# Optimization experiments

Hardware: AMD Instinct MI355X
Metric: run time of the kernel (lower is better)

Reference implementation:

```python
import jax, jax.numpy as jnp
import numpy as np
from jax import lax

BN_EPS = 1e-5

@jax.custom_vjp
def ste_sign(x):
    # Binarize to {-1, +1} (sign; 0 maps to 0 like torch.sign, negligible measure)
    return jnp.sign(x)

def _ste_fwd(x):
    return jnp.sign(x), x

def _ste_bwd(x, g):
    # Straight-through estimator: pass gradient where |x| <= 1
    return (g * (jnp.abs(x) <= 1.0).astype(g.dtype),)

ste_sign.defvjp(_ste_fwd, _ste_bwd)

def bin_conv3x3(x, w, stride=1):
    # Binarize both activations and weights, then 3x3 conv, padding=1, no bias
    xb = ste_sign(x)
    wb = ste_sign(w)
    return lax.conv_general_dilated(
        xb, wb, window_strides=(stride, stride), padding=((1, 1), (1, 1)),
        dimension_numbers=('NCHW', 'OIHW', 'NCHW'))

def batchnorm_inf(x, gamma, beta, mean, var):
    # Inference-mode BatchNorm2d over channel dim (axis=1)
    scale = gamma * lax.rsqrt(var + BN_EPS)
    shift = beta - mean * scale
    return x * scale[None, :, None, None] + shift[None, :, None, None]

def hardtanh(x):
    # SelfTanh modeled as hardtanh (standard BNN activation with STE-style grad)
    return jnp.clip(x, -1.0, 1.0)

def setup_inputs() -> dict:
    key = jax.random.key(0)
    ks = jax.random.split(key, 3)
    N, C, H, W = 64, 256, 56, 56
    x = jax.random.normal(ks[0], (N, C, H, W), dtype=jnp.float32)
    w1 = jax.random.normal(ks[1], (C, C, 3, 3), dtype=jnp.float32) * (1.0 / math_sqrt(9 * C))
    w2 = jax.random.normal(ks[2], (C, C, 3, 3), dtype=jnp.float32) * (1.0 / math_sqrt(9 * C))
    ones = jnp.ones((C,), jnp.float32)
    zeros = jnp.zeros((C,), jnp.float32)
    return {
        'x': x,
        'w1': w1, 'g1': ones, 'b1': zeros, 'm1': zeros, 'v1': ones,
        'w2': w2, 'g2': ones, 'b2': zeros, 'm2': zeros, 'v2': ones,
    }

def math_sqrt(v):
    return float(np.sqrt(v))

def reference(x, w1, g1, b1, m1, v1, w2, g2, b2, m2, v2):
    residual = x
    out = bin_conv3x3(x, w1, stride=1)
    out = batchnorm_inf(out, g1, b1, m1, v1)
    out = hardtanh(out)
    out = bin_conv3x3(out, w2, stride=1)
    out = batchnorm_inf(out, g2, b2, m2, v2)
    out = out + residual
    out = hardtanh(out)
    return out
```

## Files before the change

kernel.cpp:

```cpp
#include <hip/hip_runtime.h>
#include <stdint.h>


#define NB 64
#define C  256
#define H  56
#define W  56
#define HP 58
#define PPIX 272
#define SLOT (HP * PPIX)
#define OST 272
#define FST 116

typedef int v4i __attribute__((ext_vector_type(4)));

__global__ __launch_bounds__(256)
void pack_x_kernel(const float* __restrict__ x, int8_t* __restrict__ Aq) {
    const int h = blockIdx.x, n = blockIdx.y;
    const int w  = threadIdx.x & 63;
    const int cq = threadIdx.x >> 6;

    __shared__ int8_t st[56 * OST];

    const float* xp = x + (((size_t)n * C + cq * 64) * H + h) * W + w;
#pragma unroll
    for (int i = 0; i < 16; ++i) {
        uint32_t u = 0;
#pragma unroll
        for (int b = 0; b < 4; ++b) {
            float v = (w < 56) ? xp[(size_t)(i * 4 + b) * (H * W)] : 0.0f;
            uint32_t t = (v < 0.0f) ? 0xFFu : ((v != 0.0f) ? 1u : 0u);
            u |= t << (8 * b);
        }
        if (w < 56)
            *(uint32_t*)(st + w * OST + cq * 64 + i * 4) = u;
    }
    __syncthreads();
    int8_t* dst = Aq + (((size_t)n * HP + h + 1) * HP + 1) * C;
    for (int idx = threadIdx.x; idx < 56 * 16; idx += 256) {
        int pix = idx >> 4, c16 = idx & 15;
        *(v4i*)(dst + (size_t)pix * C + c16 * 16) =
            *(const v4i*)(st + pix * OST + c16 * 16);
    }
}

__global__ __launch_bounds__(64)
void pack_w_kernel(const float* __restrict__ wa, const float* __restrict__ wb,
                   int8_t* __restrict__ B1, int8_t* __restrict__ B2) {
    const int kstep = blockIdx.x;
    const int nfrag = blockIdx.y;
    const float* wsrc = blockIdx.z ? wb : wa;
    int8_t* dst       = blockIdx.z ? B2 : B1;
    const int lane = threadIdx.x, quad = lane >> 4, l16 = lane & 15;
    const int co = nfrag * 16 + l16;
    uint32_t pk[4];
#pragma unroll
    for (int d = 0; d < 4; ++d) {
        uint32_t u = 0;
#pragma unroll
        for (int bb = 0; bb < 4; ++bb) {
            int k = kstep * 64 + quad * 16 + d * 4 + bb;
            int tap = k >> 8, ci = k & 255;
            float v = wsrc[((size_t)co * C + ci) * 9 + tap];
            uint32_t t = (v < 0.0f) ? 0xFFu : ((v != 0.0f) ? 1u : 0u);
            u |= t << (8 * bb);
        }
        pk[d] = u;
    }
    uint4 st; st.x = pk[0]; st.y = pk[1]; st.z = pk[2]; st.w = pk[3];
    *(uint4*)(dst + ((size_t)(nfrag * 36 + kstep) * 64 + lane) * 16) = st;
}

__global__ __launch_bounds__(256)
void halo_zero_kernel(int8_t* __restrict__ Aq, int8_t* __restrict__ Bq) {
    const int n = blockIdx.x;
    int8_t* buf = blockIdx.y ? Bq : Aq;
    const v4i z = (v4i){0, 0, 0, 0};
    for (int idx = threadIdx.x; idx < 228 * 16; idx += 256) {
        int px = idx >> 4, c16 = idx & 15;
        int row, col;
        if (px < 58)       { row = 0;  col = px; }
        else if (px < 116) { row = 57; col = px - 58; }
        else { int i = px - 116; row = 1 + (i >> 1); col = (i & 1) * 57; }
        *(v4i*)(buf + (((size_t)n * HP + row) * HP + col) * C + c16 * 16) = z;
    }
}

__global__ __launch_bounds__(256)
void bn_prep_kernel(const float* g1, const float* b1, const float* m1, const float* v1,
                    const float* g2, const float* b2, const float* m2, const float* v2,
                    float* __restrict__ sc, float* __restrict__ sh) {
    const int co = threadIdx.x;
    const float* g = blockIdx.x ? g2 : g1;
    const float* b = blockIdx.x ? b2 : b1;
    const float* m = blockIdx.x ? m2 : m1;
    const float* v = blockIdx.x ? v2 : v1;
    double scd = (double)g[co] / sqrt((double)v[co] + 1e-5);
    sc[blockIdx.x * C + co] = (float)scd;
    sh[blockIdx.x * C + co] = (float)((double)b[co] - (double)m[co] * scd);
}

template <int STAGE>
__global__ __launch_bounds__(512, 4)
void mconv_kernel(const int8_t* __restrict__ Aq, const int8_t* __restrict__ Bpk,
                  const float* __restrict__ scp, const float* __restrict__ shp,
                  const float* __restrict__ resid,
                  int8_t* __restrict__ Bout, float* __restrict__ out) {
    const int h2 = blockIdx.x;
    const int n  = blockIdx.y;
    const int tid = threadIdx.x;
    const int wv = tid >> 6, lane = tid & 63, quad = lane >> 4, l16 = lane & 15;

    __shared__ int8_t lds[4 * SLOT];

    const int8_t* gA = Aq + ((size_t)n * HP + h2 * 2) * HP * C;
    for (int idx = tid; idx < 4 * HP * 16; idx += 512) {
        int pix = idx >> 4, c16 = idx & 15;
        *(v4i*)(lds + pix * PPIX + c16 * 16) =
            *(const v4i*)(gA + (size_t)pix * C + c16 * 16);
    }
    __syncthreads();

    int abase[7];
#pragma unroll
    for (int f = 0; f < 7; ++f) {
        int mm = f * 16 + l16;
        int hl = (mm >= 56) ? 1 : 0;
        int w  = mm - 56 * hl;
        abase[f] = hl * SLOT + w * PPIX + quad * 16;
    }

    const int8_t* bq0 = Bpk + (size_t)((wv * 2 + 0) * 36) * 1024 + lane * 16;
    const int8_t* bq1 = Bpk + (size_t)((wv * 2 + 1) * 36) * 1024 + lane * 16;

    v4i bcur[2];
    bcur[0] = *(const v4i*)(bq0);
    bcur[1] = *(const v4i*)(bq1);

    v4i acc[7][2];
#pragma unroll
    for (int f = 0; f < 7; ++f)
#pragma unroll
        for (int nf = 0; nf < 2; ++nf) acc[f][nf] = (v4i){0, 0, 0, 0};

#pragma unroll 1
    for (int t = 0; t < 9; ++t) {
        const int r = (t >= 6) ? 2 : ((t >= 3) ? 1 : 0);
        const int c = t - 3 * r;
        const int au = r * SLOT + c * PPIX;
#pragma unroll
        for (int ci = 0; ci < 4; ++ci) {
            v4i bn0 = *(const v4i*)(bq0 + (ci + 1) * 1024);
            v4i bn1 = *(const v4i*)(bq1 + (ci + 1) * 1024);
            v4i afr[7];
#pragma unroll
            for (int f = 0; f < 7; ++f)
                afr[f] = *(const v4i*)(lds + abase[f] + au + ci * 64);
            __builtin_amdgcn_s_setprio(1);
#pragma unroll
            for (int f = 0; f < 7; ++f) {
                acc[f][0] = __builtin_amdgcn_mfma_i32_16x16x64_i8(
                    afr[f], bcur[0], acc[f][0], 0, 0, 0);
                acc[f][1] = __builtin_amdgcn_mfma_i32_16x16x64_i8(
                    afr[f], bcur[1], acc[f][1], 0, 0, 0);
            }
            __builtin_amdgcn_s_setprio(0);
            bcur[0] = bn0;
            bcur[1] = bn1;
        }
        bq0 += 4096;
        bq1 += 4096;
    }

    if (STAGE == 1) {
        __syncthreads();
#pragma unroll
        for (int nf = 0; nf < 2; ++nf) {
            const int co = (wv * 2 + nf) * 16 + l16;
            const float scale = scp[co], shift = shp[co];
#pragma unroll
            for (int f = 0; f < 7; ++f) {
#pragma unroll
                for (int reg = 0; reg < 4; ++reg) {
                    int mm = f * 16 + quad * 4 + reg;
                    float v = __fadd_rn(__fmul_rn((float)acc[f][nf][reg], scale), shift);
                    int8_t t8 = (v < 0.0f) ? (int8_t)-1
                              : ((v != 0.0f) ? (int8_t)1 : (int8_t)0);
                    lds[mm * OST + co] = t8;
                }
            }
        }
        __syncthreads();
        for (int idx = tid; idx < 112 * 16; idx += 512) {
            int mm = idx >> 4, c16 = idx & 15;
            int hl = (mm >= 56) ? 1 : 0;
            int ww = mm - 56 * hl;
            int oh = h2 * 2 + hl;
            *(v4i*)(Bout + (((size_t)n * HP + oh + 1) * HP + ww + 1) * C + c16 * 16)
                = *(const v4i*)(lds + mm * OST + c16 * 16);
        }
    } else {
        float* fld = (float*)lds;
#pragma unroll 1
        for (int half = 0; half < 2; ++half) {
            __syncthreads();
            if ((wv >> 2) == half) {
#pragma unroll
                for (int nf = 0; nf < 2; ++nf) {
                    const int co = (wv * 2 + nf) * 16 + l16;
                    const int cop = co - half * 128;
                    const float scale = scp[co], shift = shp[co];
#pragma unroll
                    for (int f = 0; f < 7; ++f) {
                        float4 vv;
                        vv.x = __fadd_rn(__fmul_rn((float)acc[f][nf][0], scale), shift);
                        vv.y = __fadd_rn(__fmul_rn((float)acc[f][nf][1], scale), shift);
                        vv.z = __fadd_rn(__fmul_rn((float)acc[f][nf][2], scale), shift);
                        vv.w = __fadd_rn(__fmul_rn((float)acc[f][nf][3], scale), shift);
                        *(float4*)(fld + cop * FST + f * 16 + quad * 4) = vv;
                    }
                }
            }
            __syncthreads();
            for (int idx = tid; idx < 128 * 28; idx += 512) {
                int cop = idx / 28, j = idx - cop * 28;
                int row = (j >= 14) ? 1 : 0;
                int w4  = (j - row * 14) * 4;
                int mm  = row * 56 + w4;
                int co  = half * 128 + cop;
                float4 v = *(const float4*)(fld + cop * FST + mm);
                size_t gidx = (((size_t)n * C + co) * H + h2 * 2 + row) * W + w4;
                float4 rv = *(const float4*)(resid + gidx);
                float4 ov;
                ov.x = fminf(1.0f, fmaxf(-1.0f, v.x + rv.x));
                ov.y = fminf(1.0f, fmaxf(-1.0f, v.y + rv.y));
                ov.z = fminf(1.0f, fmaxf(-1.0f, v.z + rv.z));
                ov.w = fminf(1.0f, fmaxf(-1.0f, v.w + rv.w));
                *(float4*)(out + gidx) = ov;
            }
        }
    }
}

extern "C" void kernel_launch(void* const* d_in, const int* in_sizes, int n_in,
                              void* d_out, int out_size, void* d_ws, size_t ws_size,
                              hipStream_t stream) {
    const float* x  = (const float*)d_in[0];
    const float* w1 = (const float*)d_in[1];
    const float* g1 = (const float*)d_in[2];
    const float* b1 = (const float*)d_in[3];
    const float* m1 = (const float*)d_in[4];
    const float* v1 = (const float*)d_in[5];
    const float* w2 = (const float*)d_in[6];
    const float* g2 = (const float*)d_in[7];
    const float* b2 = (const float*)d_in[8];
    const float* m2 = (const float*)d_in[9];
    const float* v2 = (const float*)d_in[10];
    float* out = (float*)d_out;

    uint8_t* ws = (uint8_t*)d_ws;
    const size_t ASZ = (size_t)NB * HP * HP * C;
    const size_t WPK = (size_t)16 * 36 * 64 * 16;
    int8_t* Aq   = (int8_t*)(ws);
    int8_t* Bq   = (int8_t*)(ws + ASZ);
    int8_t* Bpk1 = (int8_t*)(ws + 2 * ASZ);
    int8_t* Bpk2 = (int8_t*)(ws + 2 * ASZ + WPK);
    float*  scb  = (float*)(ws + 2 * ASZ + 2 * WPK);
    float*  shb  = (float*)(ws + 2 * ASZ + 2 * WPK + 2048);

    halo_zero_kernel<<<dim3(NB, 2), 256, 0, stream>>>(Aq, Bq);
    bn_prep_kernel<<<dim3(2), 256, 0, stream>>>(g1, b1, m1, v1, g2, b2, m2, v2,
                                                scb, shb);
    pack_w_kernel<<<dim3(36, 16, 2), 64, 0, stream>>>(w1, w2, Bpk1, Bpk2);
    pack_x_kernel<<<dim3(H, NB), 256, 0, stream>>>(x, Aq);
    mconv_kernel<1><<<dim3(28, NB), 512, 0, stream>>>(Aq, Bpk1, scb, shb,
                                                      nullptr, Bq, nullptr);
    mconv_kernel<2><<<dim3(28, NB), 512, 0, stream>>>(Bq, Bpk2, scb + C, shb + C,
                                                      x, nullptr, out);
}
```

Measured before the change: 596.0 us.

## Process four output rows per block, reusing overlapping input rows in an LDS ring

After: 705.1 us. +18.3%, slower.

```diff
diff --git a/kernel.cpp b/kernel.cpp
--- a/kernel.cpp
+++ b/kernel.cpp
@@ -13,6 +13,14 @@
 #define FST 116
 
 typedef int v4i __attribute__((ext_vector_type(4)));
+
+__device__ __forceinline__ void wg_barrier() {
+    __builtin_amdgcn_sched_barrier(0);
+    asm volatile("s_waitcnt lgkmcnt(0)" ::: "memory");
+    __builtin_amdgcn_sched_barrier(0);
+    __builtin_amdgcn_s_barrier();
+    __builtin_amdgcn_sched_barrier(0);
+}
 
 __global__ __launch_bounds__(256)
 void pack_x_kernel(const float* __restrict__ x, int8_t* __restrict__ Aq) {
@@ -106,138 +114,164 @@
                   const float* __restrict__ scp, const float* __restrict__ shp,
                   const float* __restrict__ resid,
                   int8_t* __restrict__ Bout, float* __restrict__ out) {
-    const int h2 = blockIdx.x;
+    const int bx = blockIdx.x;
     const int n  = blockIdx.y;
     const int tid = threadIdx.x;
     const int wv = tid >> 6, lane = tid & 63, quad = lane >> 4, l16 = lane & 15;
 
     __shared__ int8_t lds[4 * SLOT];
 
-    const int8_t* gA = Aq + ((size_t)n * HP + h2 * 2) * HP * C;
-    for (int idx = tid; idx < 4 * HP * 16; idx += 512) {
-        int pix = idx >> 4, c16 = idx & 15;
-        *(v4i*)(lds + pix * PPIX + c16 * 16) =
-            *(const v4i*)(gA + (size_t)pix * C + c16 * 16);
-    }
-    __syncthreads();
-
-    int abase[7];
+    int wb[7], hlf[7];
 #pragma unroll
     for (int f = 0; f < 7; ++f) {
         int mm = f * 16 + l16;
         int hl = (mm >= 56) ? 1 : 0;
-        int w  = mm - 56 * hl;
-        abase[f] = hl * SLOT + w * PPIX + quad * 16;
-    }
-
-    const int8_t* bq0 = Bpk + (size_t)((wv * 2 + 0) * 36) * 1024 + lane * 16;
-    const int8_t* bq1 = Bpk + (size_t)((wv * 2 + 1) * 36) * 1024 + lane * 16;
-
-    v4i bcur[2];
-    bcur[0] = *(const v4i*)(bq0);
-    bcur[1] = *(const v4i*)(bq1);
-
-    v4i acc[7][2];
-#pragma unroll
-    for (int f = 0; f < 7; ++f)
-#pragma unroll
-        for (int nf = 0; nf < 2; ++nf) acc[f][nf] = (v4i){0, 0, 0, 0};
+        wb[f]  = (mm - 56 * hl) * PPIX + quad * 16;
+        hlf[f] = hl;
+    }
+
+    const int co0 = wv * 32 + l16, co1 = co0 + 16;
+    const float sc0 = scp[co0], sh0 = shp[co0];
+    const float sc1 = scp[co1], sh1 = shp[co1];
+
+    const int8_t* bq0_base = Bpk + (size_t)((wv * 2 + 0) * 36) * 1024 + lane * 16;
+    const int8_t* bq1_base = Bpk + (size_t)((wv * 2 + 1) * 36) * 1024 + lane * 16;
 
 #pragma unroll 1
-    for (int t = 0; t < 9; ++t) {
-        const int r = (t >= 6) ? 2 : ((t >= 3) ? 1 : 0);
-        const int c = t - 3 * r;
-        const int au = r * SLOT + c * PPIX;
-#pragma unroll
-        for (int ci = 0; ci < 4; ++ci) {
-            v4i bn0 = *(const v4i*)(bq0 + (ci + 1) * 1024);
-            v4i bn1 = *(const v4i*)(bq1 + (ci + 1) * 1024);
-            v4i afr[7];
-#pragma unroll
-            for (int f = 0; f < 7; ++f)
-                afr[f] = *(const v4i*)(lds + abase[f] + au + ci * 64);
-            __builtin_amdgcn_s_setprio(1);
-#pragma unroll
-            for (int f = 0; f < 7; ++f) {
-                acc[f][0] = __builtin_amdgcn_mfma_i32_16x16x64_i8(
-                    afr[f], bcur[0], acc[f][0], 0, 0, 0);
-                acc[f][1] = __builtin_amdgcn_mfma_i32_16x16x64_i8(
-                    afr[f], bcur[1], acc[f][1], 0, 0, 0);
-            }
-            __builtin_amdgcn_s_setprio(0);
-            bcur[0] = bn0;
-            bcur[1] = bn1;
-        }
-        bq0 += 4096;
-        bq1 += 4096;
-    }
-
-    if (STAGE == 1) {
-        __syncthreads();
-#pragma unroll
-        for (int nf = 0; nf < 2; ++nf) {
-            const int co = (wv * 2 + nf) * 16 + l16;
-            const float scale = scp[co], shift = shp[co];
-#pragma unroll
-            for (int f = 0; f < 7; ++f) {
-#pragma unroll
-                for (int reg = 0; reg < 4; ++reg) {
-                    int mm = f * 16 + quad * 4 + reg;
-                    float v = __fadd_rn(__fmul_rn((float)acc[f][nf][reg], scale), shift);
-                    int8_t t8 = (v < 0.0f) ? (int8_t)-1
-                              : ((v != 0.0f) ? (int8_t)1 : (int8_t)0);
-                    lds[mm * OST + co] = t8;
-                }
-            }
-        }
-        __syncthreads();
-        for (int idx = tid; idx < 112 * 16; idx += 512) {
-            int mm = idx >> 4, c16 = idx & 15;
-            int hl = (mm >= 56) ? 1 : 0;
-            int ww = mm - 56 * hl;
-            int oh = h2 * 2 + hl;
-            *(v4i*)(Bout + (((size_t)n * HP + oh + 1) * HP + ww + 1) * C + c16 * 16)
-                = *(const v4i*)(lds + mm * OST + c16 * 16);
-        }
-    } else {
-        float* fld = (float*)lds;
+    for (int tt = 0; tt < 2; ++tt) {
+        const int OH0 = 4 * bx + 2 * tt;
+
+        {
+            const int base_row = 4 * bx + (tt ? 4 : 0);
+            const int npix = (tt ? 2 : 4) * HP * 16;
+            const int8_t* gA = Aq + ((size_t)n * HP + base_row) * HP * C;
+            for (int idx = tid; idx < npix; idx += 512) {
+                int pix = idx >> 4, c16 = idx & 15;
+                *(v4i*)(lds + pix * PPIX + c16 * 16) =
+                    *(const v4i*)(gA + (size_t)pix * C + c16 * 16);
+            }
+        }
+        wg_barrier();
+
+        const int8_t* bq0 = bq0_base;
+        const int8_t* bq1 = bq1_base;
+        v4i bcur0 = *(const v4i*)bq0;
+        v4i bcur1 = *(const v4i*)bq1;
+
+        v4i acc[7][2];
+#pragma unroll
+        for (int f = 0; f < 7; ++f)
+#pragma unroll
+            for (int nf = 0; nf < 2; ++nf) acc[f][nf] = (v4i){0, 0, 0, 0};
+
 #pragma unroll 1
-        for (int half = 0; half < 2; ++half) {
-            __syncthreads();
-            if ((wv >> 2) == half) {
-#pragma unroll
-                for (int nf = 0; nf < 2; ++nf) {
-                    const int co = (wv * 2 + nf) * 16 + l16;
-                    const int cop = co - half * 128;
-                    const float scale = scp[co], shift = shp[co];
-#pragma unroll
-                    for (int f = 0; f < 7; ++f) {
-                        float4 vv;
-                        vv.x = __fadd_rn(__fmul_rn((float)acc[f][nf][0], scale), shift);
-                        vv.y = __fadd_rn(__fmul_rn((float)acc[f][nf][1], scale), shift);
-                        vv.z = __fadd_rn(__fmul_rn((float)acc[f][nf][2], scale), shift);
-                        vv.w = __fadd_rn(__fmul_rn((float)acc[f][nf][3], scale), shift);
-                        *(float4*)(fld + cop * FST + f * 16 + quad * 4) = vv;
+        for (int t9 = 0; t9 < 9; ++t9) {
+            const int r = (t9 >= 6) ? 2 : ((t9 >= 3) ? 1 : 0);
+            const int c = t9 - 3 * r;
+            const int s0 = (((tt << 1) + r) & 3) * SLOT + c * PPIX;
+            const int s1 = (((tt << 1) + r + 1) & 3) * SLOT + c * PPIX;
+            const int ds = s1 - s0;
+#pragma unroll
+            for (int ci = 0; ci < 4; ++ci) {
+                v4i bn0 = *(const v4i*)(bq0 + (ci + 1) * 1024);
+                v4i bn1 = *(const v4i*)(bq1 + (ci + 1) * 1024);
+                v4i afr[7];
+#pragma unroll
+                for (int f = 0; f < 7; ++f)
+                    afr[f] = *(const v4i*)(lds + s0 + hlf[f] * ds + wb[f] + ci * 64);
+                __builtin_amdgcn_s_setprio(1);
+#pragma unroll
+                for (int f = 0; f < 7; ++f) {
+                    acc[f][0] = __builtin_amdgcn_mfma_i32_16x16x64_i8(
+                        afr[f], bcur0, acc[f][0], 0, 0, 0);
+                    acc[f][1] = __builtin_amdgcn_mfma_i32_16x16x64_i8(
+                        afr[f], bcur1, acc[f][1], 0, 0, 0);
+                }
+                __builtin_amdgcn_s_setprio(0);
+                bcur0 = bn0;
+                bcur1 = bn1;
+            }
+            bq0 += 4096;
+            bq1 += 4096;
+        }
+
+        if (STAGE == 1) {
+            wg_barrier();
+#pragma unroll
+            for (int nf = 0; nf < 2; ++nf) {
+                const int co = wv * 32 + nf * 16 + l16;
+                const float scale = nf ? sc1 : sc0;
+                const float shift = nf ? sh1 : sh0;
+#pragma unroll
+                for (int f = 0; f < 7; ++f) {
+#pragma unroll
+                    for (int reg = 0; reg < 4; ++reg) {
+                        int mm = f * 16 + quad * 4 + reg;
+                        float v = __fadd_rn(__fmul_rn((float)acc[f][nf][reg], scale), shift);
+                        int8_t t8 = (v < 0.0f) ? (int8_t)-1
+                                  : ((v != 0.0f) ? (int8_t)1 : (int8_t)0);
+                        lds[mm * OST + co] = t8;
                     }
                 }
             }
-            __syncthreads();
-            for (int idx = tid; idx < 128 * 28; idx += 512) {
-                int cop = idx / 28, j = idx - cop * 28;
-                int row = (j >= 14) ? 1 : 0;
-                int w4  = (j - row * 14) * 4;
-                int mm  = row * 56 + w4;
-                int co  = half * 128 + cop;
-                float4 v = *(const float4*)(fld + cop * FST + mm);
-                size_t gidx = (((size_t)n * C + co) * H + h2 * 2 + row) * W + w4;
-                float4 rv = *(const float4*)(resid + gidx);
-                float4 ov;
-                ov.x = fminf(1.0f, fmaxf(-1.0f, v.x + rv.x));
-                ov.y = fminf(1.0f, fmaxf(-1.0f, v.y + rv.y));
-                ov.z = fminf(1.0f, fmaxf(-1.0f, v.z + rv.z));
-                ov.w = fminf(1.0f, fmaxf(-1.0f, v.w + rv.w));
-                *(float4*)(out + gidx) = ov;
-            }
+            wg_barrier();
+#pragma unroll
+            for (int k = 0; k < 4; ++k) {
+                int idx = tid + k * 512;
+                if (idx < 112 * 16) {
+                    int mm = idx >> 4, c16 = idx & 15;
+                    int hl = (mm >= 56) ? 1 : 0;
+                    int ww = mm - 56 * hl;
+                    int oh = OH0 + hl;
+                    *(v4i*)(Bout + (((size_t)n * HP + oh + 1) * HP + ww + 1) * C + c16 * 16)
+                        = *(const v4i*)(lds + mm * OST + c16 * 16);
+                }
+            }
+            wg_barrier();
+        } else {
+            float* fld = (float*)lds;
+#pragma unroll 1
+            for (int qtr = 0; qtr < 4; ++qtr) {
+                wg_barrier();
+                if ((wv >> 1) == qtr) {
+#pragma unroll
+                    for (int nf = 0; nf < 2; ++nf) {
+                        const int cop = (wv * 32 + nf * 16 + l16) & 63;
+                        const float scale = nf ? sc1 : sc0;
+                        const float shift = nf ? sh1 : sh0;
+#pragma unroll
+                        for (int f = 0; f < 7; ++f) {
+                            float4 vv;
+                            vv.x = __fadd_rn(__fmul_rn((float)acc[f][nf][0], scale), shift);
+                            vv.y = __fadd_rn(__fmul_rn((float)acc[f][nf][1], scale), shift);
+                            vv.z = __fadd_rn(__fmul_rn((float)acc[f][nf][2], scale), shift);
+                            vv.w = __fadd_rn(__fmul_rn((float)acc[f][nf][3], scale), shift);
+                            *(float4*)(fld + cop * FST + f * 16 + quad * 4) = vv;
+                        }
+                    }
+                }
+                wg_barrier();
+#pragma unroll
+                for (int k = 0; k < 4; ++k) {
+                    int idx = tid + k * 512;
+                    if (idx < 64 * 28) {
+                        int cop = idx / 28, j = idx - cop * 28;
+                        int row = (j >= 14) ? 1 : 0;
+                        int w4  = (j - row * 14) * 4;
+                        int co  = qtr * 64 + cop;
+                        float4 v = *(const float4*)(fld + cop * FST + row * 56 + w4);
+                        size_t gidx = (((size_t)n * C + co) * H + OH0 + row) * W + w4;
+                        float4 rv = *(const float4*)(resid + gidx);
+                        float4 ov;
+                        ov.x = fminf(1.0f, fmaxf(-1.0f, v.x + rv.x));
+                        ov.y = fminf(1.0f, fmaxf(-1.0f, v.y + rv.y));
+                        ov.z = fminf(1.0f, fmaxf(-1.0f, v.z + rv.z));
+                        ov.w = fminf(1.0f, fmaxf(-1.0f, v.w + rv.w));
+                        *(float4*)(out + gidx) = ov;
+                    }
+                }
+            }
+            wg_barrier();
         }
     }
 }
@@ -273,8 +307,8 @@
                                                 scb, shb);
     pack_w_kernel<<<dim3(36, 16, 2), 64, 0, stream>>>(w1, w2, Bpk1, Bpk2);
     pack_x_kernel<<<dim3(H, NB), 256, 0, stream>>>(x, Aq);
-    mconv_kernel<1><<<dim3(28, NB), 512, 0, stream>>>(Aq, Bpk1, scb, shb,
+    mconv_kernel<1><<<dim3(14, NB), 512, 0, stream>>>(Aq, Bpk1, scb, shb,
                                                       nullptr, Bq, nullptr);
-    mconv_kernel<2><<<dim3(28, NB), 512, 0, stream>>>(Bq, Bpk2, scb + C, shb + C,
+    mconv_kernel<2><<<dim3(14, NB), 512, 0, stream>>>(Bq, Bpk2, scb + C, shb + C,
                                                       x, nullptr, out);
 }
```

## Retile conv waves into a 2x4 grid of pixel and channel fragments

Applied to the files above, without the earlier changes.

After: 638.6 us. 1.07x slower.

```diff
diff --git a/kernel.cpp b/kernel.cpp
--- a/kernel.cpp
+++ b/kernel.cpp
@@ -100,6 +100,43 @@
     sh[blockIdx.x * C + co] = (float)((double)b[co] - (double)m[co] * scd);
 }
 
+template <int MF>
+__device__ __forceinline__ void kloop(const int8_t* __restrict__ lds8,
+                                      const int (&abase)[4],
+                                      const int8_t* __restrict__ b0,
+                                      const int8_t* __restrict__ b1,
+                                      const int8_t* __restrict__ b2,
+                                      const int8_t* __restrict__ b3,
+                                      v4i (&acc)[4][4]) {
+#pragma unroll 1
+    for (int t = 0; t < 9; ++t) {
+        const int r = (t >= 6) ? 2 : ((t >= 3) ? 1 : 0);
+        const int c = t - 3 * r;
+        const int au = r * SLOT + c * PPIX;
+#pragma unroll
+        for (int ci = 0; ci < 4; ++ci) {
+            v4i bf[4];
+            bf[0] = *(const v4i*)(b0 + ci * 1024);
+            bf[1] = *(const v4i*)(b1 + ci * 1024);
+            bf[2] = *(const v4i*)(b2 + ci * 1024);
+            bf[3] = *(const v4i*)(b3 + ci * 1024);
+            v4i afr[MF];
+#pragma unroll
+            for (int f = 0; f < MF; ++f)
+                afr[f] = *(const v4i*)(lds8 + abase[f] + au + ci * 64);
+            __builtin_amdgcn_s_setprio(1);
+#pragma unroll
+            for (int f = 0; f < MF; ++f)
+#pragma unroll
+                for (int nf = 0; nf < 4; ++nf)
+                    acc[f][nf] = __builtin_amdgcn_mfma_i32_16x16x64_i8(
+                        afr[f], bf[nf], acc[f][nf], 0, 0, 0);
+            __builtin_amdgcn_s_setprio(0);
+        }
+        b0 += 4096; b1 += 4096; b2 += 4096; b3 += 4096;
+    }
+}
+
 template <int STAGE>
 __global__ __launch_bounds__(512, 4)
 void mconv_kernel(const int8_t* __restrict__ Aq, const int8_t* __restrict__ Bpk,
@@ -110,6 +147,7 @@
     const int n  = blockIdx.y;
     const int tid = threadIdx.x;
     const int wv = tid >> 6, lane = tid & 63, quad = lane >> 4, l16 = lane & 15;
+    const int wrow = wv >> 2, wcol = wv & 3;
 
     __shared__ int8_t lds[4 * SLOT];
 
@@ -121,72 +159,47 @@
     }
     __syncthreads();
 
-    int abase[7];
-#pragma unroll
-    for (int f = 0; f < 7; ++f) {
-        int mm = f * 16 + l16;
+    int abase[4];
+#pragma unroll
+    for (int f = 0; f < 4; ++f) {
+        int fg = wrow * 4 + f;
+        if (fg > 6) fg = 6;
+        int mm = fg * 16 + l16;
         int hl = (mm >= 56) ? 1 : 0;
-        int w  = mm - 56 * hl;
-        abase[f] = hl * SLOT + w * PPIX + quad * 16;
-    }
-
-    const int8_t* bq0 = Bpk + (size_t)((wv * 2 + 0) * 36) * 1024 + lane * 16;
-    const int8_t* bq1 = Bpk + (size_t)((wv * 2 + 1) * 36) * 1024 + lane * 16;
-
-    v4i bcur[2];
-    bcur[0] = *(const v4i*)(bq0);
-    bcur[1] = *(const v4i*)(bq1);
-
-    v4i acc[7][2];
-#pragma unroll
-    for (int f = 0; f < 7; ++f)
-#pragma unroll
-        for (int nf = 0; nf < 2; ++nf) acc[f][nf] = (v4i){0, 0, 0, 0};
-
-#pragma unroll 1
-    for (int t = 0; t < 9; ++t) {
-        const int r = (t >= 6) ? 2 : ((t >= 3) ? 1 : 0);
-        const int c = t - 3 * r;
-        const int au = r * SLOT + c * PPIX;
-#pragma unroll
-        for (int ci = 0; ci < 4; ++ci) {
-            v4i bn0 = *(const v4i*)(bq0 + (ci + 1) * 1024);
-            v4i bn1 = *(const v4i*)(bq1 + (ci + 1) * 1024);
-            v4i afr[7];
-#pragma unroll
-            for (int f = 0; f < 7; ++f)
-                afr[f] = *(const v4i*)(lds + abase[f] + au + ci * 64);
-            __builtin_amdgcn_s_setprio(1);
-#pragma unroll
-            for (int f = 0; f < 7; ++f) {
-                acc[f][0] = __builtin_amdgcn_mfma_i32_16x16x64_i8(
-                    afr[f], bcur[0], acc[f][0], 0, 0, 0);
-                acc[f][1] = __builtin_amdgcn_mfma_i32_16x16x64_i8(
-                    afr[f], bcur[1], acc[f][1], 0, 0, 0);
-            }
-            __builtin_amdgcn_s_setprio(0);
-            bcur[0] = bn0;
-            bcur[1] = bn1;
-        }
-        bq0 += 4096;
-        bq1 += 4096;
-    }
+        abase[f] = hl * SLOT + (mm - 56 * hl) * PPIX + quad * 16;
+    }
+
+    const int8_t* b0 = Bpk + (size_t)((wcol * 4 + 0) * 36) * 1024 + lane * 16;
+    const int8_t* b1 = Bpk + (size_t)((wcol * 4 + 1) * 36) * 1024 + lane * 16;
+    const int8_t* b2 = Bpk + (size_t)((wcol * 4 + 2) * 36) * 1024 + lane * 16;
+    const int8_t* b3 = Bpk + (size_t)((wcol * 4 + 3) * 36) * 1024 + lane * 16;
+
+    v4i acc[4][4];
+#pragma unroll
+    for (int f = 0; f < 4; ++f)
+#pragma unroll
+        for (int nf = 0; nf < 4; ++nf) acc[f][nf] = (v4i){0, 0, 0, 0};
+
+    if (wrow == 0) kloop<4>(lds, abase, b0, b1, b2, b3, acc);
+    else           kloop<3>(lds, abase, b0, b1, b2, b3, acc);
 
     if (STAGE == 1) {
         __syncthreads();
 #pragma unroll
-        for (int nf = 0; nf < 2; ++nf) {
-            const int co = (wv * 2 + nf) * 16 + l16;
+        for (int nf = 0; nf < 4; ++nf) {
+            const int co = (wcol * 4 + nf) * 16 + l16;
             const float scale = scp[co], shift = shp[co];
 #pragma unroll
-            for (int f = 0; f < 7; ++f) {
-#pragma unroll
-                for (int reg = 0; reg < 4; ++reg) {
-                    int mm = f * 16 + quad * 4 + reg;
-                    float v = __fadd_rn(__fmul_rn((float)acc[f][nf][reg], scale), shift);
-                    int8_t t8 = (v < 0.0f) ? (int8_t)-1
-                              : ((v != 0.0f) ? (int8_t)1 : (int8_t)0);
-                    lds[mm * OST + co] = t8;
+            for (int f = 0; f < 4; ++f) {
+                if (f < 3 || wrow == 0) {
+                    const int mmb = (wrow * 4 + f) * 16 + quad * 4;
+#pragma unroll
+                    for (int reg = 0; reg < 4; ++reg) {
+                        float v = __fadd_rn(__fmul_rn((float)acc[f][nf][reg], scale), shift);
+                        int8_t t8 = (v < 0.0f) ? (int8_t)-1
+                                  : ((v != 0.0f) ? (int8_t)1 : (int8_t)0);
+                        lds[(mmb + reg) * OST + co] = t8;
+                    }
                 }
             }
         }
@@ -204,20 +217,23 @@
 #pragma unroll 1
         for (int half = 0; half < 2; ++half) {
             __syncthreads();
-            if ((wv >> 2) == half) {
-#pragma unroll
-                for (int nf = 0; nf < 2; ++nf) {
-                    const int co = (wv * 2 + nf) * 16 + l16;
-                    const int cop = co - half * 128;
+            if ((wcol >> 1) == half) {
+                const int copb = (wcol & 1) * 64;
+#pragma unroll
+                for (int nf = 0; nf < 4; ++nf) {
+                    const int cop = copb + nf * 16 + l16;
+                    const int co  = half * 128 + cop;
                     const float scale = scp[co], shift = shp[co];
 #pragma unroll
-                    for (int f = 0; f < 7; ++f) {
-                        float4 vv;
-                        vv.x = __fadd_rn(__fmul_rn((float)acc[f][nf][0], scale), shift);
-                        vv.y = __fadd_rn(__fmul_rn((float)acc[f][nf][1], scale), shift);
-                        vv.z = __fadd_rn(__fmul_rn((float)acc[f][nf][2], scale), shift);
-                        vv.w = __fadd_rn(__fmul_rn((float)acc[f][nf][3], scale), shift);
-                        *(float4*)(fld + cop * FST + f * 16 + quad * 4) = vv;
+                    for (int f = 0; f < 4; ++f) {
+                        if (f < 3 || wrow == 0) {
+                            float4 vv;
+                            vv.x = __fadd_rn(__fmul_rn((float)acc[f][nf][0], scale), shift);
+                            vv.y = __fadd_rn(__fmul_rn((float)acc[f][nf][1], scale), shift);
+                            vv.z = __fadd_rn(__fmul_rn((float)acc[f][nf][2], scale), shift);
+                            vv.w = __fadd_rn(__fmul_rn((float)acc[f][nf][3], scale), shift);
+                            *(float4*)(fld + cop * FST + (wrow * 4 + f) * 16 + quad * 4) = vv;
+                        }
                     }
                 }
             }
```
